# Kernel optimization log

Hardware: AMD Instinct MI355X
Metric: run time of the kernel (lower is better)

The kernel has to match this reference:

```python
import jax, jax.numpy as jnp
import numpy as np
from jax import lax

D_MODEL = 1024
D_STATE = 16
D_CONV = 4
EXPAND = 2
D_INNER = EXPAND * D_MODEL          # 2048
DT_RANK = D_MODEL // 16             # 64 (mamba default 'auto')
B, L = 2, 2048
EPS = 1e-5


def setup_inputs() -> dict:
    key = jax.random.key(0)
    ks = jax.random.split(key, 8)
    def nrm(k, shape, scale=0.02):
        return jax.random.normal(k, shape, jnp.float32) * scale
    x = jax.random.normal(ks[0], (B, L, D_MODEL), jnp.float32)
    gamma = jnp.ones((D_MODEL,), jnp.float32)
    beta = jnp.zeros((D_MODEL,), jnp.float32)
    W_in = nrm(ks[1], (2 * D_INNER, D_MODEL))                      # in_proj, no bias
    conv_w = nrm(ks[2], (D_INNER, D_CONV), 0.1)                    # depthwise conv
    conv_b = jnp.zeros((D_INNER,), jnp.float32)
    W_x = nrm(ks[3], (DT_RANK + 2 * D_STATE, D_INNER))             # x_proj, no bias
    W_dt = nrm(ks[4], (D_INNER, DT_RANK), 0.1)                     # dt_proj
    b_dt = jnp.log(jnp.expm1(jnp.full((D_INNER,), 0.01, jnp.float32)))  # softplus(b_dt)=0.01
    # S4D-real init: A[d, n] = n+1
    A_log = jnp.log(jnp.tile(jnp.arange(1, D_STATE + 1, dtype=jnp.float32), (D_INNER, 1)))
    D_param = jnp.ones((D_INNER,), jnp.float32)
    W_out = nrm(ks[5], (D_MODEL, D_INNER))                         # out_proj, no bias
    return {"x": x, "gamma": gamma, "beta": beta, "W_in": W_in,
            "conv_w": conv_w, "conv_b": conv_b, "W_x": W_x,
            "W_dt": W_dt, "b_dt": b_dt, "A_log": A_log,
            "D_param": D_param, "W_out": W_out}


def _layernorm(x, gamma, beta):
    mu = jnp.mean(x, axis=-1, keepdims=True)
    var = jnp.mean(jnp.square(x - mu), axis=-1, keepdims=True)
    return (x - mu) * lax.rsqrt(var + EPS) * gamma + beta


def _mamba_block(x, gamma, beta, W_in, conv_w, conv_b, W_x, W_dt, b_dt, A_log, D_param, W_out):
    xn = _layernorm(x, gamma, beta)                                # [B,L,Dm]
    xz = jnp.einsum('bld,ed->ble', xn, W_in)                       # [B,L,2*Di]
    u, z = jnp.split(xz, 2, axis=-1)                               # each [B,L,Di]
    # depthwise causal conv over the sequence dim
    u_ncl = jnp.transpose(u, (0, 2, 1))                            # [B,Di,L]
    kern = conv_w[:, None, :]                                      # [Di,1,K]
    u_conv = lax.conv_general_dilated(
        u_ncl, kern, window_strides=(1,), padding=[(D_CONV - 1, 0)],
        feature_group_count=D_INNER,
        dimension_numbers=('NCH', 'OIH', 'NCH')) + conv_b[None, :, None]
    u_conv = jax.nn.silu(jnp.transpose(u_conv, (0, 2, 1)))         # [B,L,Di]
    # input-dependent dt, B, C
    x_dbl = jnp.einsum('bld,ed->ble', u_conv, W_x)                 # [B,L,R+2N]
    dt_r = x_dbl[..., :DT_RANK]
    Bmat = x_dbl[..., DT_RANK:DT_RANK + D_STATE]                   # [B,L,N]
    Cmat = x_dbl[..., DT_RANK + D_STATE:]                          # [B,L,N]
    dt = jax.nn.softplus(jnp.einsum('blr,dr->bld', dt_r, W_dt) + b_dt)  # [B,L,Di]
    A = -jnp.exp(A_log)                                            # [Di,N]
    dA = jnp.exp(jnp.einsum('bld,dn->bldn', dt, A))                # [B,L,Di,N]
    dBu = (dt * u_conv)[..., None] * Bmat[:, :, None, :]           # [B,L,Di,N]
    # selective scan, time-major
    dA_t = jnp.moveaxis(dA, 1, 0)                                  # [L,B,Di,N]
    dBu_t = jnp.moveaxis(dBu, 1, 0)
    C_t = jnp.moveaxis(Cmat, 1, 0)                                 # [L,B,N]
    def step(h, inp):
        dA_i, dBu_i, C_i = inp
        h = dA_i * h + dBu_i                                       # [B,Di,N]
        y = jnp.einsum('bdn,bn->bd', h, C_i)                       # [B,Di]
        return h, y
    h0 = jnp.zeros((x.shape[0], D_INNER, D_STATE), x.dtype)
    _, ys = lax.scan(step, h0, (dA_t, dBu_t, C_t))                 # [L,B,Di]
    y = jnp.moveaxis(ys, 0, 1) + u_conv * D_param                  # [B,L,Di]
    y = y * jax.nn.silu(z)                                         # gate
    upd = jnp.einsum('bld,ed->ble', y, W_out)                      # [B,L,Dm]
    return x + upd                                                 # residual (dropout=0 -> Identity)


def reference(x, gamma, beta, W_in, conv_w, conv_b, W_x, W_dt, b_dt, A_log, D_param, W_out):
    return _mamba_block(x, gamma, beta, W_in, conv_w, conv_b, W_x, W_dt, b_dt, A_log, D_param, W_out)
```

## Files before the change

kernel.cpp:

```cpp
#include <hip/hip_runtime.h>
#include <hip/hip_bf16.h>
#include <math.h>

#define D_MODEL 1024
#define D_STATE 16
#define D_INNER 2048
#define DT_RANK 64
#define BATCH   2
#define SEQLEN  2048
#define NTOK    4096
#define XDBL_W  96
#define CHUNK   64
#define NCHUNK  32

typedef unsigned short u16;
typedef __attribute__((ext_vector_type(8))) short bf16x8;
typedef __attribute__((ext_vector_type(4))) float f32x4;

__device__ __forceinline__ u16 f2b(float f) {
    __hip_bfloat16 h = __float2bfloat16(f);
    union { __hip_bfloat16 h; u16 u; } cv; cv.h = h; return cv.u;
}
__device__ __forceinline__ float b2f(u16 u) {
    union { unsigned u; float f; } cv; cv.u = ((unsigned)u) << 16; return cv.f;
}

__device__ __forceinline__ void gload16(const u16* g, u16* l) {
    __builtin_amdgcn_global_load_lds((const __attribute__((address_space(1))) void*)g,
                                     (__attribute__((address_space(3))) void*)l, 16, 0, 0);
}

__global__ __launch_bounds__(256) void cvt_all(
    const float* __restrict__ s0, u16* __restrict__ d0, int n0,
    const float* __restrict__ s1, u16* __restrict__ d1, int n1,
    const float* __restrict__ s2, u16* __restrict__ d2, int n2,
    const float* __restrict__ s3, u16* __restrict__ d3, int n3) {
    int i = (blockIdx.x * 256 + threadIdx.x) * 4;
    const float* s; u16* d;
    if (i < n0)                { s = s0 + i; d = d0 + i; }
    else if ((i -= n0) < n1)   { s = s1 + i; d = d1 + i; }
    else if ((i -= n1) < n2)   { s = s2 + i; d = d2 + i; }
    else if ((i -= n2) < n3)   { s = s3 + i; d = d3 + i; }
    else return;
    float4 v = *(const float4*)s;
    ushort4 o;
    o.x = f2b(v.x); o.y = f2b(v.y); o.z = f2b(v.z); o.w = f2b(v.w);
    *(ushort4*)d = o;
}

__global__ __launch_bounds__(256) void cvt_dtr(const float* __restrict__ xdbl,
                                               u16* __restrict__ dtrb) {
    const int i = blockIdx.x * 256 + threadIdx.x;
    const int row = i >> 4, c4 = (i & 15) * 4;
    float4 v = *(const float4*)&xdbl[(size_t)row * XDBL_W + c4];
    ushort4 o;
    o.x = f2b(v.x); o.y = f2b(v.y); o.z = f2b(v.z); o.w = f2b(v.w);
    *(ushort4*)&dtrb[(size_t)row * DT_RANK + c4] = o;
}

__global__ __launch_bounds__(256) void zerof(float* __restrict__ p, int n) {
    const int i = blockIdx.x * 256 + threadIdx.x;
    if (i < n) p[i] = 0.0f;
}

__global__ __launch_bounds__(256) void ln_kernel(const float* __restrict__ x,
                                                 const float* __restrict__ g,
                                                 const float* __restrict__ be,
                                                 u16* __restrict__ xnb) {
    __shared__ float sh[8];
    const int t = blockIdx.x;
    float4 v = ((const float4*)(x + (size_t)t * D_MODEL))[threadIdx.x];
    float s  = v.x + v.y + v.z + v.w;
    float ss = v.x * v.x + v.y * v.y + v.z * v.z + v.w * v.w;
#pragma unroll
    for (int o = 32; o > 0; o >>= 1) {
        s  += __shfl_down(s,  o, 64);
        ss += __shfl_down(ss, o, 64);
    }
    const int wid = threadIdx.x >> 6;
    if ((threadIdx.x & 63) == 0) { sh[wid * 2] = s; sh[wid * 2 + 1] = ss; }
    __syncthreads();
    s  = sh[0] + sh[2] + sh[4] + sh[6];
    ss = sh[1] + sh[3] + sh[5] + sh[7];
    const float mu  = s * (1.0f / D_MODEL);
    const float var = ss * (1.0f / D_MODEL) - mu * mu;
    const float inv = rsqrtf(var + 1e-5f);
    float4 gv = ((const float4*)g)[threadIdx.x];
    float4 bv = ((const float4*)be)[threadIdx.x];
    ushort4 o;
    o.x = f2b((v.x - mu) * inv * gv.x + bv.x);
    o.y = f2b((v.y - mu) * inv * gv.y + bv.y);
    o.z = f2b((v.z - mu) * inv * gv.z + bv.z);
    o.w = f2b((v.w - mu) * inv * gv.w + bv.w);
    ((ushort4*)(xnb + (size_t)t * D_MODEL))[threadIdx.x] = o;
}

__global__ __launch_bounds__(512, 1) void gemm256(
    const u16* __restrict__ A, const u16* __restrict__ Bm,
    u16* __restrict__ Cout, int N, int K, int nbx) {
    __shared__ u16 lds[4 * 16384];
    int bid = blockIdx.x;
    { const int cpx = gridDim.x >> 3; bid = (bid & 7) * cpx + (bid >> 3); }
    const int bm = (bid / nbx) * 256, bn = (bid % nbx) * 256;
    const int t = threadIdx.x;
    const int lane = t & 63;
    const int wv = t >> 6, wr = wv >> 2, wc = wv & 3;
    const int fr = lane & 15, fq = lane >> 4;
    const int NT = K >> 5;
    const int srow = t >> 2;
    const int scol = ((t & 3) ^ (srow & 3)) * 8;
    const u16* ga0 = A  + (size_t)(bm + srow) * K + scol;
    const u16* ga1 = A  + (size_t)(bm + srow + 128) * K + scol;
    const u16* gb0 = Bm + (size_t)(bn + srow) * K + scol;
    const u16* gb1 = Bm + (size_t)(bn + srow + 128) * K + scol;
    int aoff[8], boff[4];
#pragma unroll
    for (int i = 0; i < 8; ++i) {
        const int r = wr * 128 + i * 16 + fr;
        aoff[i] = r * 32 + ((fq ^ (r & 3)) * 8);
    }
#pragma unroll
    for (int j = 0; j < 4; ++j) {
        const int r = wc * 64 + j * 16 + fr;
        boff[j] = 8192 + r * 32 + ((fq ^ (r & 3)) * 8);
    }
    f32x4 acc[8][4] = {};

#define STG(tt) { u16* s_ = &lds[((tt) & 3) * 16384]; const size_t ko = (size_t)(tt) * 32; \
        gload16(ga0 + ko, s_ + t * 8); \
        gload16(ga1 + ko, s_ + 4096 + t * 8); \
        gload16(gb0 + ko, s_ + 8192 + t * 8); \
        gload16(gb1 + ko, s_ + 12288 + t * 8); }

    STG(0); STG(1); STG(2);
    asm volatile("s_waitcnt vmcnt(8)" ::: "memory");
    __builtin_amdgcn_s_barrier();
    __builtin_amdgcn_sched_barrier(0);

    for (int kt = 0; kt < NT; ++kt) {
        if (kt + 3 < NT) STG(kt + 3);
        const u16* S = &lds[(kt & 3) * 16384];
        bf16x8 bf[4];
#pragma unroll
        for (int j = 0; j < 4; ++j) bf[j] = *(const bf16x8*)&S[boff[j]];
#pragma unroll
        for (int ih = 0; ih < 2; ++ih) {
            bf16x8 af[4];
#pragma unroll
            for (int i2 = 0; i2 < 4; ++i2) af[i2] = *(const bf16x8*)&S[aoff[ih * 4 + i2]];
            __builtin_amdgcn_s_setprio(1);
#pragma unroll
            for (int i2 = 0; i2 < 4; ++i2)
#pragma unroll
                for (int j = 0; j < 4; ++j)
                    acc[ih * 4 + i2][j] =
                        __builtin_amdgcn_mfma_f32_16x16x32_bf16(af[i2], bf[j], acc[ih * 4 + i2][j], 0, 0, 0);
            __builtin_amdgcn_s_setprio(0);
        }
        if (kt + 1 < NT) {
            const int cnt = (kt + 3 <= NT - 1) ? 3 : (NT - 1 - kt);
            if (cnt == 3)      asm volatile("s_waitcnt vmcnt(8)" ::: "memory");
            else if (cnt == 2) asm volatile("s_waitcnt vmcnt(4)" ::: "memory");
            else               asm volatile("s_waitcnt vmcnt(0)" ::: "memory");
            __builtin_amdgcn_s_barrier();
            __builtin_amdgcn_sched_barrier(0);
        }
    }
#undef STG

#pragma unroll
    for (int i = 0; i < 8; ++i) {
        const int row0 = bm + wr * 128 + i * 16 + fq * 4;
#pragma unroll
        for (int j = 0; j < 4; ++j) {
            const int col = bn + wc * 64 + j * 16 + fr;
#pragma unroll
            for (int r = 0; r < 4; ++r)
                Cout[(size_t)(row0 + r) * N + col] = f2b(acc[i][j][r]);
        }
    }
}

template<int MODE>
__global__ __launch_bounds__(512, 1) void gemm_ring(
    const u16* __restrict__ A, const u16* __restrict__ Bm,
    const float* __restrict__ resid, void* __restrict__ Cout,
    int N, int K, int nbx) {
    __shared__ u16 lds[4 * 8192];
    const int nwg = gridDim.x;
    int bid = blockIdx.x;
    { const int cpx = nwg >> 3; bid = (bid & 7) * cpx + (bid >> 3); }
    const int bx = bid % nbx, by = bid / nbx;
    const int bm = by * 128, bn = bx * 128;
    const int t = threadIdx.x;
    const int lane = t & 63;
    const int wv = t >> 6, wr = wv >> 2, wc = wv & 3;
    const int fr = lane & 15, fq = lane >> 4;
    const int NT = K >> 5;
    const int srow = t >> 2;
    const int scol = ((t & 3) ^ ((t >> 3) & 3)) * 8;
    const u16* ga = A  + (size_t)(bm + srow) * K + scol;
    const u16* gb = Bm + (size_t)(bn + srow) * K + scol;
    const int sw = (fq ^ ((fr >> 1) & 3)) * 8;
    f32x4 acc[4][2] = {};

#define ISSUE(tt) { u16* s_ = &lds[((tt) & 3) * 8192]; \
        gload16(ga + (size_t)(tt) * 32, s_ + t * 8); \
        gload16(gb + (size_t)(tt) * 32, s_ + 4096 + t * 8); }

    ISSUE(0); if (NT > 1) ISSUE(1); if (NT > 2) ISSUE(2);
    if (NT > 2)      asm volatile("s_waitcnt vmcnt(4)" ::: "memory");
    else if (NT > 1) asm volatile("s_waitcnt vmcnt(2)" ::: "memory");
    else             asm volatile("s_waitcnt vmcnt(0)" ::: "memory");
    __builtin_amdgcn_s_barrier();
    __builtin_amdgcn_sched_barrier(0);

    for (int tt = 0; tt < NT; ++tt) {
        if (tt + 3 < NT) ISSUE(tt + 3);
        const u16* As = &lds[(tt & 3) * 8192];
        const u16* Bs = As + 4096;
        bf16x8 af[4], bfv[2];
#pragma unroll
        for (int j = 0; j < 2; ++j)
            bfv[j] = *(const bf16x8*)&Bs[(wc * 32 + j * 16 + fr) * 32 + sw];
#pragma unroll
        for (int i = 0; i < 4; ++i)
            af[i] = *(const bf16x8*)&As[(wr * 64 + i * 16 + fr) * 32 + sw];
        __builtin_amdgcn_s_setprio(1);
#pragma unroll
        for (int i = 0; i < 4; ++i)
#pragma unroll
            for (int j = 0; j < 2; ++j)
                acc[i][j] = __builtin_amdgcn_mfma_f32_16x16x32_bf16(af[i], bfv[j], acc[i][j], 0, 0, 0);
        __builtin_amdgcn_s_setprio(0);
        if (tt + 1 < NT) {
            const int it = (tt + 3 < NT) ? (tt + 3) : (NT - 1);
            const int rem = it - (tt + 1);
            if (rem >= 2)      asm volatile("s_waitcnt vmcnt(4)" ::: "memory");
            else if (rem == 1) asm volatile("s_waitcnt vmcnt(2)" ::: "memory");
            else               asm volatile("s_waitcnt vmcnt(0)" ::: "memory");
            __builtin_amdgcn_s_barrier();
            __builtin_amdgcn_sched_barrier(0);
        }
    }
#undef ISSUE

#pragma unroll
    for (int i = 0; i < 4; ++i) {
        const int row0 = bm + wr * 64 + i * 16 + fq * 4;
#pragma unroll
        for (int j = 0; j < 2; ++j) {
            const int col = bn + wc * 32 + j * 16 + fr;
#pragma unroll
            for (int r = 0; r < 4; ++r) {
                const size_t idx = (size_t)(row0 + r) * N + col;
                if (MODE == 1) {
                    ((float*)Cout)[idx] = acc[i][j][r] + resid[idx];
                } else {
                    const float v = acc[i][j][r] + resid[col];
                    const float sp = (v > 20.0f) ? v : log1pf(__expf(v));
                    ((u16*)Cout)[idx] = f2b(sp);
                }
            }
        }
    }
}

__global__ __launch_bounds__(256) void gemm_splitk(
    const u16* __restrict__ A, const u16* __restrict__ Bm,
    float* __restrict__ Cout, int ldc, int Nvalid, int K, int kpb) {
    __shared__ u16 As[128 * 32];
    __shared__ u16 Bs[128 * 32];
    const int t = threadIdx.x;
    const int bm = blockIdx.y * 128, bn = blockIdx.x * 128;
    const int kbeg = blockIdx.z * kpb, kend = kbeg + kpb;
    const int sr = t >> 2, sc = (t & 3) * 8;
    const int lane = t & 63, wv = t >> 6;
    const int wr = wv >> 1, wc = wv & 1;
    const int fr = lane & 15, fq = lane >> 4;
    int br0 = bn + sr;      if (br0 > Nvalid - 1) br0 = Nvalid - 1;
    int br1 = bn + 64 + sr; if (br1 > Nvalid - 1) br1 = Nvalid - 1;
    const u16* Ar0 = A + (size_t)(bm + sr) * K;
    const u16* Ar1 = A + (size_t)(bm + 64 + sr) * K;
    const u16* Br0 = Bm + (size_t)br0 * K;
    const u16* Br1 = Bm + (size_t)br1 * K;
    f32x4 acc[4][4] = {};
    for (int k0 = kbeg; k0 < kend; k0 += 32) {
        gload16(Ar0 + k0 + sc, &As[t * 8]);
        gload16(Ar1 + k0 + sc, &As[2048 + t * 8]);
        gload16(Br0 + k0 + sc, &Bs[t * 8]);
        gload16(Br1 + k0 + sc, &Bs[2048 + t * 8]);
        asm volatile("s_waitcnt vmcnt(0)" ::: "memory");
        __syncthreads();
        bf16x8 af[4], bfv[4];
#pragma unroll
        for (int i = 0; i < 4; ++i)
            af[i] = *(const bf16x8*)&As[(wr * 64 + i * 16 + fr) * 32 + fq * 8];
#pragma unroll
        for (int j = 0; j < 4; ++j)
            bfv[j] = *(const bf16x8*)&Bs[(wc * 64 + j * 16 + fr) * 32 + fq * 8];
#pragma unroll
        for (int i = 0; i < 4; ++i)
#pragma unroll
            for (int j = 0; j < 4; ++j)
                acc[i][j] = __builtin_amdgcn_mfma_f32_16x16x32_bf16(af[i], bfv[j], acc[i][j], 0, 0, 0);
        __syncthreads();
    }
#pragma unroll
    for (int i = 0; i < 4; ++i) {
        const int row0 = bm + wr * 64 + i * 16 + fq * 4;
#pragma unroll
        for (int j = 0; j < 4; ++j) {
            const int col = bn + wc * 64 + j * 16 + fr;
            if (col < Nvalid) {
#pragma unroll
                for (int r = 0; r < 4; ++r)
                    atomicAdd(&Cout[(size_t)(row0 + r) * ldc + col], acc[i][j][r]);
            }
        }
    }
}

__global__ __launch_bounds__(256) void conv_silu(const u16* __restrict__ xzb,
                                                 const float* __restrict__ cw,
                                                 const float* __restrict__ cb,
                                                 u16* __restrict__ ucb) {
    const int i4 = blockIdx.x * 256 + threadIdx.x;
    const int dq = i4 & 511;
    const int tok = i4 >> 9;
    const int l = tok & (SEQLEN - 1);
    const int d = dq * 4;
    const size_t base = ((size_t)tok << 12) + d;
    const ushort4 zz = {0, 0, 0, 0};
    ushort4 t0 = (l >= 3) ? *(const ushort4*)&xzb[base - 3 * 4096] : zz;
    ushort4 t1 = (l >= 2) ? *(const ushort4*)&xzb[base - 2 * 4096] : zz;
    ushort4 t2 = (l >= 1) ? *(const ushort4*)&xzb[base - 1 * 4096] : zz;
    ushort4 t3 = *(const ushort4*)&xzb[base];
    ushort4 o;
    {
        float4 w = *(const float4*)&cw[(d + 0) * 4];
        float s = cb[d + 0] + b2f(t0.x) * w.x + b2f(t1.x) * w.y + b2f(t2.x) * w.z + b2f(t3.x) * w.w;
        o.x = f2b(s / (1.0f + __expf(-s)));
    }
    {
        float4 w = *(const float4*)&cw[(d + 1) * 4];
        float s = cb[d + 1] + b2f(t0.y) * w.x + b2f(t1.y) * w.y + b2f(t2.y) * w.z + b2f(t3.y) * w.w;
        o.y = f2b(s / (1.0f + __expf(-s)));
    }
    {
        float4 w = *(const float4*)&cw[(d + 2) * 4];
        float s = cb[d + 2] + b2f(t0.z) * w.x + b2f(t1.z) * w.y + b2f(t2.z) * w.z + b2f(t3.z) * w.w;
        o.z = f2b(s / (1.0f + __expf(-s)));
    }
    {
        float4 w = *(const float4*)&cw[(d + 3) * 4];
        float s = cb[d + 3] + b2f(t0.w) * w.x + b2f(t1.w) * w.y + b2f(t2.w) * w.z + b2f(t3.w) * w.w;
        o.w = f2b(s / (1.0f + __expf(-s)));
    }
    *(ushort4*)&ucb[(size_t)tok * D_INNER + d] = o;
}


__global__ __launch_bounds__(256) void scan_phase1(const u16* __restrict__ dtb,
                                                   const u16* __restrict__ ucb,
                                                   const float* __restrict__ xdbl,
                                                   float* __restrict__ SH,
                                                   float* __restrict__ sumdt) {
    const int d = blockIdx.x * 256 + threadIdx.x;
    const int c = blockIdx.y, b = blockIdx.z;
    const int tok0 = b * SEQLEN + c * CHUNK;
    __shared__ float Bsh[CHUNK][D_STATE];
    {
        const int i = threadIdx.x;
        const int row = i >> 2, c4 = (i & 3) * 4;
        *(float4*)&Bsh[row][c4] = *(const float4*)&xdbl[(size_t)(tok0 + row) * XDBL_W + DT_RANK + c4];
    }
    __syncthreads();
    float h[D_STATE];
#pragma unroll
    for (int n = 0; n < D_STATE; ++n) h[n] = 0.0f;
    float sd = 0.0f;
    float dtv = b2f(dtb[(size_t)tok0 * D_INNER + d]);
    float uv  = b2f(ucb[(size_t)tok0 * D_INNER + d]);
    for (int l = 0; l < CHUNK; ++l) {
        float ndt = 0.0f, nu = 0.0f;
        if (l < CHUNK - 1) {
            ndt = b2f(dtb[(size_t)(tok0 + l + 1) * D_INNER + d]);
            nu  = b2f(ucb[(size_t)(tok0 + l + 1) * D_INNER + d]);
        }
        sd += dtv;
        const float dtu = dtv * uv;
        const float q = __expf(-dtv);
        const float* Bl = Bsh[l];
        float dA = 1.0f;
#pragma unroll
        for (int n = 0; n < D_STATE; ++n) {
            dA *= q;
            h[n] = fmaf(dA, h[n], dtu * Bl[n]);
        }
        dtv = ndt; uv = nu;
    }
    const size_t sidx = (size_t)(b * NCHUNK + c) * D_INNER + d;
#pragma unroll
    for (int n4 = 0; n4 < 4; ++n4) {
        float4 o; o.x = h[n4 * 4]; o.y = h[n4 * 4 + 1]; o.z = h[n4 * 4 + 2]; o.w = h[n4 * 4 + 3];
        *(float4*)&SH[sidx * D_STATE + n4 * 4] = o;
    }
    sumdt[sidx] = sd;
}

__global__ __launch_bounds__(256) void scan_combine(const float* __restrict__ sumdt,
                                                    float* __restrict__ SH) {
    const int d = blockIdx.x * 256 + threadIdx.x;
    const int b = blockIdx.y;
    float H[D_STATE];
#pragma unroll
    for (int n = 0; n < D_STATE; ++n) H[n] = 0.0f;
    for (int c = 0; c < NCHUNK; ++c) {
        const size_t sidx = (size_t)(b * NCHUNK + c) * D_INNER + d;
        float S[D_STATE];
#pragma unroll
        for (int n4 = 0; n4 < 4; ++n4) {
            float4 sv = *(const float4*)&SH[sidx * D_STATE + n4 * 4];
            S[n4 * 4] = sv.x; S[n4 * 4 + 1] = sv.y; S[n4 * 4 + 2] = sv.z; S[n4 * 4 + 3] = sv.w;
        }
        const float qq = __expf(-sumdt[sidx]);
#pragma unroll
        for (int n4 = 0; n4 < 4; ++n4) {
            float4 o; o.x = H[n4 * 4]; o.y = H[n4 * 4 + 1]; o.z = H[n4 * 4 + 2]; o.w = H[n4 * 4 + 3];
            *(float4*)&SH[sidx * D_STATE + n4 * 4] = o;
        }
        float dA = 1.0f;
#pragma unroll
        for (int n = 0; n < D_STATE; ++n) {
            dA *= qq;
            H[n] = fmaf(dA, H[n], S[n]);
        }
    }
}

__global__ __launch_bounds__(256) void scan_phase3(const u16* __restrict__ dtb,
                                                   const u16* __restrict__ ucb,
                                                   const float* __restrict__ xdbl,
                                                   const float* __restrict__ Dp,
                                                   const u16* __restrict__ xzb,
                                                   const float* __restrict__ SH,
                                                   u16* __restrict__ ybf) {
    const int d = blockIdx.x * 256 + threadIdx.x;
    const int c = blockIdx.y, b = blockIdx.z;
    const int tok0 = b * SEQLEN + c * CHUNK;
    __shared__ float Bsh[CHUNK][D_STATE];
    __shared__ float Csh[CHUNK][D_STATE];
    {
        const int i = threadIdx.x;
        const int row = i >> 2, c4 = (i & 3) * 4;
        *(float4*)&Bsh[row][c4] = *(const float4*)&xdbl[(size_t)(tok0 + row) * XDBL_W + DT_RANK + c4];
        *(float4*)&Csh[row][c4] = *(const float4*)&xdbl[(size_t)(tok0 + row) * XDBL_W + DT_RANK + D_STATE + c4];
    }
    __syncthreads();
    const float Dpv = Dp[d];
    const size_t sidx = (size_t)(b * NCHUNK + c) * D_INNER + d;
    float h[D_STATE];
#pragma unroll
    for (int n4 = 0; n4 < 4; ++n4) {
        float4 hv = *(const float4*)&SH[sidx * D_STATE + n4 * 4];
        h[n4 * 4] = hv.x; h[n4 * 4 + 1] = hv.y; h[n4 * 4 + 2] = hv.z; h[n4 * 4 + 3] = hv.w;
    }
    float dtv = b2f(dtb[(size_t)tok0 * D_INNER + d]);
    float uv  = b2f(ucb[(size_t)tok0 * D_INNER + d]);
    float zv  = b2f(xzb[((size_t)tok0 << 12) + D_INNER + d]);
    for (int l = 0; l < CHUNK; ++l) {
        float ndt = 0.0f, nu = 0.0f, nz = 0.0f;
        if (l < CHUNK - 1) {
            const size_t t2 = tok0 + l + 1;
            ndt = b2f(dtb[t2 * D_INNER + d]);
            nu  = b2f(ucb[t2 * D_INNER + d]);
            nz  = b2f(xzb[(t2 << 12) + D_INNER + d]);
        }
        const float dtu = dtv * uv;
        const float q = __expf(-dtv);
        const float* Bl = Bsh[l];
        const float* Cl = Csh[l];
        float yv = 0.0f;
        float dA = 1.0f;
#pragma unroll
        for (int n = 0; n < D_STATE; ++n) {
            dA *= q;
            h[n] = fmaf(dA, h[n], dtu * Bl[n]);
            yv = fmaf(h[n], Cl[n], yv);
        }
        yv = fmaf(uv, Dpv, yv);
        const float g = zv / (1.0f + __expf(-zv));
        ybf[(size_t)(tok0 + l) * D_INNER + d] = f2b(yv * g);
        dtv = ndt; uv = nu; zv = nz;
    }
}

extern "C" void kernel_launch(void* const* d_in, const int* in_sizes, int n_in,
                              void* d_out, int out_size, void* d_ws, size_t ws_size,
                              hipStream_t stream) {
    const float* x      = (const float*)d_in[0];
    const float* gamma  = (const float*)d_in[1];
    const float* beta   = (const float*)d_in[2];
    const float* W_in   = (const float*)d_in[3];
    const float* conv_w = (const float*)d_in[4];
    const float* conv_b = (const float*)d_in[5];
    const float* W_x    = (const float*)d_in[6];
    const float* W_dt   = (const float*)d_in[7];
    const float* b_dt   = (const float*)d_in[8];
    const float* D_par  = (const float*)d_in[10];
    const float* W_out  = (const float*)d_in[11];
    float* out = (float*)d_out;

    char* p = (char*)d_ws;
    u16* xnb   = (u16*)p;  p += (size_t)NTOK * D_MODEL * 2;
    u16* Winb  = (u16*)p;  p += (size_t)2 * D_INNER * D_MODEL * 2;
    u16* ybf   = xnb;
    u16* Woutb = (u16*)p;  p += (size_t)D_MODEL * D_INNER * 2;
    u16* Wxb   = (u16*)p;  p += (size_t)XDBL_W * D_INNER * 2;
    u16* Wdtb  = (u16*)p;  p += (size_t)D_INNER * DT_RANK * 2;
    u16* dtrb  = (u16*)p;  p += (size_t)NTOK * DT_RANK * 2;
    u16* xzb   = (u16*)p;  p += (size_t)NTOK * 2 * D_INNER * 2;
    u16* ucb   = (u16*)p;  p += (size_t)NTOK * D_INNER * 2;
    u16* dtb   = (u16*)p;  p += (size_t)NTOK * D_INNER * 2;
    float* xdbl  = (float*)p; p += (size_t)NTOK * XDBL_W * 4;
    float* sumdt = (float*)p; p += (size_t)BATCH * NCHUNK * D_INNER * 4;
    float* SH    = (float*)p; p += (size_t)BATCH * NCHUNK * D_INNER * D_STATE * 4;

    {
        const int n0 = 2 * D_INNER * D_MODEL, n1 = D_MODEL * D_INNER,
                  n2 = XDBL_W * D_INNER, n3 = D_INNER * DT_RANK;
        const int tot = (n0 + n1 + n2 + n3) / 4;
        cvt_all<<<(tot + 255) / 256, 256, 0, stream>>>(W_in, Winb, n0, W_out, Woutb, n1,
                                                       W_x, Wxb, n2, W_dt, Wdtb, n3);
    }

    ln_kernel<<<NTOK, 256, 0, stream>>>(x, gamma, beta, xnb);

    gemm256<<<256, 512, 0, stream>>>(xnb, Winb, xzb, 4096, 1024, 16);

    conv_silu<<<NTOK * 512 / 256, 256, 0, stream>>>(xzb, conv_w, conv_b, ucb);

    zerof<<<(NTOK * XDBL_W + 255) / 256, 256, 0, stream>>>(xdbl, NTOK * XDBL_W);
    gemm_splitk<<<dim3(1, 32, 4), 256, 0, stream>>>(ucb, Wxb, xdbl,
                                                    XDBL_W, XDBL_W, 2048, 512);

    cvt_dtr<<<256, 256, 0, stream>>>(xdbl, dtrb);
    gemm_ring<2><<<512, 512, 0, stream>>>(dtrb, Wdtb, b_dt, dtb, 2048, 64, 16);

    scan_phase1<<<dim3(8, NCHUNK, BATCH), 256, 0, stream>>>(dtb, ucb, xdbl, SH, sumdt);
    scan_combine<<<dim3(8, BATCH, 1), 256, 0, stream>>>(sumdt, SH);
    scan_phase3<<<dim3(8, NCHUNK, BATCH), 256, 0, stream>>>(dtb, ucb, xdbl, D_par,
                                                            xzb, SH, ybf);

    gemm_ring<1><<<256, 512, 0, stream>>>(ybf, Woutb, x, out, 1024, 2048, 8);
}
```

Baseline: 236.4 us.

## Fuse LN, weight conversion and zeroing; add BK=64 out-proj GEMM; change swizzle

Merges layernorm, the bf16 weight conversion and the xdbl zero-fill into a single prep launch, which removes two kernel launches. Adds a dedicated out-projection GEMM with a K-tile of 64, an 8-way XOR swizzle and a 3-stage LDS ring, giving fewer barriers per K. Also changes the LDS swizzle pattern in gemm256 to cut bank conflicts. The larger LDS footprint and the new swizzle carry some correctness and occupancy risk.

```diff
diff --git a/kernel.cpp b/kernel.cpp
--- a/kernel.cpp
+++ b/kernel.cpp
@@ -30,22 +30,59 @@
                                      (__attribute__((address_space(3))) void*)l, 16, 0, 0);
 }
 
-__global__ __launch_bounds__(256) void cvt_all(
+#define CVT_BLKS 6464
+#define ZERO_BLKS 1536
+__global__ __launch_bounds__(256) void prep(
+    const float* __restrict__ x, const float* __restrict__ g, const float* __restrict__ be,
+    u16* __restrict__ xnb,
     const float* __restrict__ s0, u16* __restrict__ d0, int n0,
     const float* __restrict__ s1, u16* __restrict__ d1, int n1,
     const float* __restrict__ s2, u16* __restrict__ d2, int n2,
-    const float* __restrict__ s3, u16* __restrict__ d3, int n3) {
-    int i = (blockIdx.x * 256 + threadIdx.x) * 4;
-    const float* s; u16* d;
-    if (i < n0)                { s = s0 + i; d = d0 + i; }
-    else if ((i -= n0) < n1)   { s = s1 + i; d = d1 + i; }
-    else if ((i -= n1) < n2)   { s = s2 + i; d = d2 + i; }
-    else if ((i -= n2) < n3)   { s = s3 + i; d = d3 + i; }
-    else return;
-    float4 v = *(const float4*)s;
-    ushort4 o;
-    o.x = f2b(v.x); o.y = f2b(v.y); o.z = f2b(v.z); o.w = f2b(v.w);
-    *(ushort4*)d = o;
+    const float* __restrict__ s3, u16* __restrict__ d3, int n3,
+    float* __restrict__ xdbl) {
+    const int bid = blockIdx.x;
+    if (bid < NTOK) {
+        __shared__ float sh[8];
+        float4 v = ((const float4*)(x + (size_t)bid * D_MODEL))[threadIdx.x];
+        float s  = v.x + v.y + v.z + v.w;
+        float ss = v.x * v.x + v.y * v.y + v.z * v.z + v.w * v.w;
+#pragma unroll
+        for (int o = 32; o > 0; o >>= 1) {
+            s  += __shfl_down(s,  o, 64);
+            ss += __shfl_down(ss, o, 64);
+        }
+        const int wid = threadIdx.x >> 6;
+        if ((threadIdx.x & 63) == 0) { sh[wid * 2] = s; sh[wid * 2 + 1] = ss; }
+        __syncthreads();
+        s  = sh[0] + sh[2] + sh[4] + sh[6];
+        ss = sh[1] + sh[3] + sh[5] + sh[7];
+        const float mu  = s * (1.0f / D_MODEL);
+        const float var = ss * (1.0f / D_MODEL) - mu * mu;
+        const float inv = rsqrtf(var + 1e-5f);
+        float4 gv = ((const float4*)g)[threadIdx.x];
+        float4 bv = ((const float4*)be)[threadIdx.x];
+        ushort4 o;
+        o.x = f2b((v.x - mu) * inv * gv.x + bv.x);
+        o.y = f2b((v.y - mu) * inv * gv.y + bv.y);
+        o.z = f2b((v.z - mu) * inv * gv.z + bv.z);
+        o.w = f2b((v.w - mu) * inv * gv.w + bv.w);
+        ((ushort4*)(xnb + (size_t)bid * D_MODEL))[threadIdx.x] = o;
+    } else if (bid < NTOK + CVT_BLKS) {
+        int i = ((bid - NTOK) * 256 + threadIdx.x) * 4;
+        const float* s; u16* d;
+        if (i < n0)                { s = s0 + i; d = d0 + i; }
+        else if ((i -= n0) < n1)   { s = s1 + i; d = d1 + i; }
+        else if ((i -= n1) < n2)   { s = s2 + i; d = d2 + i; }
+        else if ((i -= n2) < n3)   { s = s3 + i; d = d3 + i; }
+        else return;
+        float4 v = *(const float4*)s;
+        ushort4 o;
+        o.x = f2b(v.x); o.y = f2b(v.y); o.z = f2b(v.z); o.w = f2b(v.w);
+        *(ushort4*)d = o;
+    } else {
+        const int j = (bid - NTOK - CVT_BLKS) * 256 + threadIdx.x;
+        if (j < NTOK * XDBL_W) xdbl[j] = 0.0f;
+    }
 }
 
 __global__ __launch_bounds__(256) void cvt_dtr(const float* __restrict__ xdbl,
@@ -56,43 +93,6 @@
     ushort4 o;
     o.x = f2b(v.x); o.y = f2b(v.y); o.z = f2b(v.z); o.w = f2b(v.w);
     *(ushort4*)&dtrb[(size_t)row * DT_RANK + c4] = o;
-}
-
-__global__ __launch_bounds__(256) void zerof(float* __restrict__ p, int n) {
-    const int i = blockIdx.x * 256 + threadIdx.x;
-    if (i < n) p[i] = 0.0f;
-}
-
-__global__ __launch_bounds__(256) void ln_kernel(const float* __restrict__ x,
-                                                 const float* __restrict__ g,
-                                                 const float* __restrict__ be,
-                                                 u16* __restrict__ xnb) {
-    __shared__ float sh[8];
-    const int t = blockIdx.x;
-    float4 v = ((const float4*)(x + (size_t)t * D_MODEL))[threadIdx.x];
-    float s  = v.x + v.y + v.z + v.w;
-    float ss = v.x * v.x + v.y * v.y + v.z * v.z + v.w * v.w;
-#pragma unroll
-    for (int o = 32; o > 0; o >>= 1) {
-        s  += __shfl_down(s,  o, 64);
-        ss += __shfl_down(ss, o, 64);
-    }
-    const int wid = threadIdx.x >> 6;
-    if ((threadIdx.x & 63) == 0) { sh[wid * 2] = s; sh[wid * 2 + 1] = ss; }
-    __syncthreads();
-    s  = sh[0] + sh[2] + sh[4] + sh[6];
-    ss = sh[1] + sh[3] + sh[5] + sh[7];
-    const float mu  = s * (1.0f / D_MODEL);
-    const float var = ss * (1.0f / D_MODEL) - mu * mu;
-    const float inv = rsqrtf(var + 1e-5f);
-    float4 gv = ((const float4*)g)[threadIdx.x];
-    float4 bv = ((const float4*)be)[threadIdx.x];
-    ushort4 o;
-    o.x = f2b((v.x - mu) * inv * gv.x + bv.x);
-    o.y = f2b((v.y - mu) * inv * gv.y + bv.y);
-    o.z = f2b((v.z - mu) * inv * gv.z + bv.z);
-    o.w = f2b((v.w - mu) * inv * gv.w + bv.w);
-    ((ushort4*)(xnb + (size_t)t * D_MODEL))[threadIdx.x] = o;
 }
 
 __global__ __launch_bounds__(512, 1) void gemm256(
@@ -108,22 +108,17 @@
     const int fr = lane & 15, fq = lane >> 4;
     const int NT = K >> 5;
     const int srow = t >> 2;
-    const int scol = ((t & 3) ^ (srow & 3)) * 8;
+    const int scol = ((t & 3) ^ ((t >> 3) & 3)) * 8;
     const u16* ga0 = A  + (size_t)(bm + srow) * K + scol;
     const u16* ga1 = A  + (size_t)(bm + srow + 128) * K + scol;
     const u16* gb0 = Bm + (size_t)(bn + srow) * K + scol;
     const u16* gb1 = Bm + (size_t)(bn + srow + 128) * K + scol;
+    const int rsw = (fq ^ ((fr >> 1) & 3)) * 8;
     int aoff[8], boff[4];
 #pragma unroll
-    for (int i = 0; i < 8; ++i) {
-        const int r = wr * 128 + i * 16 + fr;
-        aoff[i] = r * 32 + ((fq ^ (r & 3)) * 8);
-    }
-#pragma unroll
-    for (int j = 0; j < 4; ++j) {
-        const int r = wc * 64 + j * 16 + fr;
-        boff[j] = 8192 + r * 32 + ((fq ^ (r & 3)) * 8);
-    }
+    for (int i = 0; i < 8; ++i) aoff[i] = (wr * 128 + i * 16 + fr) * 32 + rsw;
+#pragma unroll
+    for (int j = 0; j < 4; ++j) boff[j] = 8192 + (wc * 64 + j * 16 + fr) * 32 + rsw;
     f32x4 acc[8][4] = {};
 
 #define STG(tt) { u16* s_ = &lds[((tt) & 3) * 16384]; const size_t ko = (size_t)(tt) * 32; \
@@ -181,17 +176,108 @@
     }
 }
 
-template<int MODE>
-__global__ __launch_bounds__(512, 1) void gemm_ring(
+__global__ __launch_bounds__(512, 1) void gemm_out(
     const u16* __restrict__ A, const u16* __restrict__ Bm,
-    const float* __restrict__ resid, void* __restrict__ Cout,
+    const float* __restrict__ resid, float* __restrict__ Cout,
+    int N, int K, int nbx) {
+    __shared__ u16 lds[3 * 16384];
+    int bid = blockIdx.x;
+    { const int cpx = gridDim.x >> 3; bid = (bid & 7) * cpx + (bid >> 3); }
+    const int bm = (bid / nbx) * 128, bn = (bid % nbx) * 128;
+    const int t = threadIdx.x;
+    const int lane = t & 63;
+    const int wv = t >> 6, wr = wv >> 2, wc = wv & 3;
+    const int fr = lane & 15, fq = lane >> 4;
+    const int NT = K >> 6;
+    const int srow = t >> 3;
+    const int scol = ((t & 7) ^ ((t >> 3) & 7)) * 8;
+    const u16* ga0 = A  + (size_t)(bm + srow) * K + scol;
+    const u16* ga1 = A  + (size_t)(bm + srow + 64) * K + scol;
+    const u16* gb0 = Bm + (size_t)(bn + srow) * K + scol;
+    const u16* gb1 = Bm + (size_t)(bn + srow + 64) * K + scol;
+    int aoff[4][2], boff[2][2];
+#pragma unroll
+    for (int i = 0; i < 4; ++i) {
+        const int r = wr * 64 + i * 16 + fr;
+#pragma unroll
+        for (int ks = 0; ks < 2; ++ks)
+            aoff[i][ks] = r * 64 + (((ks * 4 + fq) ^ (fr & 7)) * 8);
+    }
+#pragma unroll
+    for (int j = 0; j < 2; ++j) {
+        const int r = wc * 32 + j * 16 + fr;
+#pragma unroll
+        for (int ks = 0; ks < 2; ++ks)
+            boff[j][ks] = 8192 + r * 64 + (((ks * 4 + fq) ^ (fr & 7)) * 8);
+    }
+    f32x4 acc[4][2] = {};
+
+#define STG2(ss, kt) { u16* s_ = &lds[(ss) * 16384]; const size_t ko = (size_t)(kt) * 64; \
+        gload16(ga0 + ko, s_ + t * 8); \
+        gload16(ga1 + ko, s_ + 4096 + t * 8); \
+        gload16(gb0 + ko, s_ + 8192 + t * 8); \
+        gload16(gb1 + ko, s_ + 12288 + t * 8); }
+
+    STG2(0, 0); STG2(1, 1);
+    asm volatile("s_waitcnt vmcnt(4)" ::: "memory");
+    __builtin_amdgcn_s_barrier();
+    __builtin_amdgcn_sched_barrier(0);
+
+    int sl = 0;
+    for (int kt = 0; kt < NT; ++kt) {
+        if (kt + 2 < NT) {
+            int s2 = sl + 2; if (s2 >= 3) s2 -= 3;
+            STG2(s2, kt + 2);
+        }
+        const u16* S = &lds[sl * 16384];
+#pragma unroll
+        for (int ks = 0; ks < 2; ++ks) {
+            bf16x8 af[4], bfv[2];
+#pragma unroll
+            for (int j = 0; j < 2; ++j) bfv[j] = *(const bf16x8*)&S[boff[j][ks]];
+#pragma unroll
+            for (int i = 0; i < 4; ++i) af[i] = *(const bf16x8*)&S[aoff[i][ks]];
+            __builtin_amdgcn_s_setprio(1);
+#pragma unroll
+            for (int i = 0; i < 4; ++i)
+#pragma unroll
+                for (int j = 0; j < 2; ++j)
+                    acc[i][j] = __builtin_amdgcn_mfma_f32_16x16x32_bf16(af[i], bfv[j], acc[i][j], 0, 0, 0);
+            __builtin_amdgcn_s_setprio(0);
+        }
+        if (kt + 1 < NT) {
+            if (kt + 2 < NT) asm volatile("s_waitcnt vmcnt(4)" ::: "memory");
+            else             asm volatile("s_waitcnt vmcnt(0)" ::: "memory");
+            __builtin_amdgcn_s_barrier();
+            __builtin_amdgcn_sched_barrier(0);
+        }
+        sl = (sl == 2) ? 0 : sl + 1;
+    }
+#undef STG2
+
+#pragma unroll
+    for (int i = 0; i < 4; ++i) {
+        const int row0 = bm + wr * 64 + i * 16 + fq * 4;
+#pragma unroll
+        for (int j = 0; j < 2; ++j) {
+            const int col = bn + wc * 32 + j * 16 + fr;
+#pragma unroll
+            for (int r = 0; r < 4; ++r) {
+                const size_t idx = (size_t)(row0 + r) * N + col;
+                Cout[idx] = acc[i][j][r] + resid[idx];
+            }
+        }
+    }
+}
+
+__global__ __launch_bounds__(512, 1) void gemm_dt(
+    const u16* __restrict__ A, const u16* __restrict__ Bm,
+    const float* __restrict__ bias, u16* __restrict__ Cout,
     int N, int K, int nbx) {
     __shared__ u16 lds[4 * 8192];
-    const int nwg = gridDim.x;
     int bid = blockIdx.x;
-    { const int cpx = nwg >> 3; bid = (bid & 7) * cpx + (bid >> 3); }
-    const int bx = bid % nbx, by = bid / nbx;
-    const int bm = by * 128, bn = bx * 128;
+    { const int cpx = gridDim.x >> 3; bid = (bid & 7) * cpx + (bid >> 3); }
+    const int bm = (bid / nbx) * 128, bn = (bid % nbx) * 128;
     const int t = threadIdx.x;
     const int lane = t & 63;
     const int wv = t >> 6, wr = wv >> 2, wc = wv & 3;
@@ -253,14 +339,9 @@
             const int col = bn + wc * 32 + j * 16 + fr;
 #pragma unroll
             for (int r = 0; r < 4; ++r) {
-                const size_t idx = (size_t)(row0 + r) * N + col;
-                if (MODE == 1) {
-                    ((float*)Cout)[idx] = acc[i][j][r] + resid[idx];
-                } else {
-                    const float v = acc[i][j][r] + resid[col];
-                    const float sp = (v > 20.0f) ? v : log1pf(__expf(v));
-                    ((u16*)Cout)[idx] = f2b(sp);
-                }
+                const float v = acc[i][j][r] + bias[col];
+                const float sp = (v > 20.0f) ? v : log1pf(__expf(v));
+                Cout[(size_t)(row0 + r) * N + col] = f2b(sp);
             }
         }
     }
@@ -530,28 +611,25 @@
     {
         const int n0 = 2 * D_INNER * D_MODEL, n1 = D_MODEL * D_INNER,
                   n2 = XDBL_W * D_INNER, n3 = D_INNER * DT_RANK;
-        const int tot = (n0 + n1 + n2 + n3) / 4;
-        cvt_all<<<(tot + 255) / 256, 256, 0, stream>>>(W_in, Winb, n0, W_out, Woutb, n1,
-                                                       W_x, Wxb, n2, W_dt, Wdtb, n3);
-    }
-
-    ln_kernel<<<NTOK, 256, 0, stream>>>(x, gamma, beta, xnb);
+        prep<<<NTOK + CVT_BLKS + ZERO_BLKS, 256, 0, stream>>>(
+            x, gamma, beta, xnb,
+            W_in, Winb, n0, W_out, Woutb, n1, W_x, Wxb, n2, W_dt, Wdtb, n3, xdbl);
+    }
 
     gemm256<<<256, 512, 0, stream>>>(xnb, Winb, xzb, 4096, 1024, 16);
 
     conv_silu<<<NTOK * 512 / 256, 256, 0, stream>>>(xzb, conv_w, conv_b, ucb);
 
-    zerof<<<(NTOK * XDBL_W + 255) / 256, 256, 0, stream>>>(xdbl, NTOK * XDBL_W);
     gemm_splitk<<<dim3(1, 32, 4), 256, 0, stream>>>(ucb, Wxb, xdbl,
                                                     XDBL_W, XDBL_W, 2048, 512);
 
     cvt_dtr<<<256, 256, 0, stream>>>(xdbl, dtrb);
-    gemm_ring<2><<<512, 512, 0, stream>>>(dtrb, Wdtb, b_dt, dtb, 2048, 64, 16);
+    gemm_dt<<<512, 512, 0, stream>>>(dtrb, Wdtb, b_dt, dtb, 2048, 64, 16);
 
     scan_phase1<<<dim3(8, NCHUNK, BATCH), 256, 0, stream>>>(dtb, ucb, xdbl, SH, sumdt);
     scan_combine<<<dim3(8, BATCH, 1), 256, 0, stream>>>(sumdt, SH);
     scan_phase3<<<dim3(8, NCHUNK, BATCH), 256, 0, stream>>>(dtb, ucb, xdbl, D_par,
                                                             xzb, SH, ybf);
 
-    gemm_ring<1><<<256, 512, 0, stream>>>(ybf, Woutb, x, out, 1024, 2048, 8);
-}
+    gemm_out<<<256, 512, 0, stream>>>(ybf, Woutb, x, out, 1024, 2048, 8);
+}
```

Result: faster. 231.1 us (-2.3%).
